# Performance work log

Measured on AMD Instinct MI355X. Metric: run time of the kernel, lower is better.

Reference implementation:

```python
import jax, jax.numpy as jnp
import numpy as np

K = 3; PAD = 1; STRIDE = 1; EPS = 1e-5


def setup_inputs() -> dict:
    key = jax.random.key(0)
    k0, k1, k2 = jax.random.split(key, 3)
    B, C, H, W, O = 4, 256, 64, 64, 256
    x = jax.random.normal(k0, (B, C, H, W), jnp.float32)
    # offset conv: small random weights so offsets are nontrivial but bounded
    w_off = jax.random.normal(k1, (2 * K * K, C, K, K), jnp.float32) * 0.01
    b_off = jnp.zeros((2 * K * K,), jnp.float32)
    # kaiming normal, mode=fan_out: std = sqrt(2 / (O*K*K))
    w_def = jax.random.normal(k2, (O, C, K, K), jnp.float32) * np.float32(np.sqrt(2.0 / (O * K * K)))
    gamma = jnp.ones((O,), jnp.float32)
    beta = jnp.zeros((O,), jnp.float32)
    return {"x": x, "w_off": w_off, "b_off": b_off, "w_def": w_def, "gamma": gamma, "beta": beta}


def _bilinear_gather(x, py, px):
    """x: [B,C,H,W]; py,px: [B,K2,Ho,Wo] float sample coords.
    Returns [B,K2,Ho,Wo,C] with zero padding outside (per-corner masking,
    matching torchvision deform_conv2d)."""
    B, C, H, W = x.shape
    y0f = jnp.floor(py); x0f = jnp.floor(px)
    wy1 = py - y0f; wy0 = 1.0 - wy1
    wx1 = px - x0f; wx0 = 1.0 - wx1
    bidx = jnp.arange(B)[:, None, None, None]

    def corner(yf, xf, wgt):
        valid = (yf >= 0) & (yf <= H - 1) & (xf >= 0) & (xf <= W - 1)
        yc = jnp.clip(yf.astype(jnp.int32), 0, H - 1)
        xc = jnp.clip(xf.astype(jnp.int32), 0, W - 1)
        v = x[bidx, :, yc, xc]  # [B,K2,Ho,Wo,C] (advanced idx moves C last)
        return v * (wgt * valid)[..., None]

    return (corner(y0f, x0f, wy0 * wx0) + corner(y0f, x0f + 1.0, wy0 * wx1)
            + corner(y0f + 1.0, x0f, wy1 * wx0) + corner(y0f + 1.0, x0f + 1.0, wy1 * wx1))


def _forward(x, w_off, b_off, w_def, gamma, beta):
    B, C, H, W = x.shape
    O = w_def.shape[0]
    K2 = K * K
    # 1) offset-predicting conv
    off = jax.lax.conv_general_dilated(x, w_off, (STRIDE, STRIDE), ((PAD, PAD), (PAD, PAD)))
    off = off + b_off[None, :, None, None]
    Ho, Wo = off.shape[2], off.shape[3]
    off = off.reshape(B, K2, 2, Ho, Wo)  # pairs (dy, dx) per kernel tap
    # 2) deformable sampling locations
    ky, kx = jnp.meshgrid(jnp.arange(K, dtype=jnp.float32), jnp.arange(K, dtype=jnp.float32), indexing='ij')
    base_y = (jnp.arange(Ho, dtype=jnp.float32) * STRIDE - PAD)
    base_x = (jnp.arange(Wo, dtype=jnp.float32) * STRIDE - PAD)
    py = off[:, :, 0] + ky.reshape(K2)[None, :, None, None] + base_y[None, None, :, None]
    px = off[:, :, 1] + kx.reshape(K2)[None, :, None, None] + base_x[None, None, None, :]
    vals = _bilinear_gather(x, py, px)  # [B,K2,Ho,Wo,C]
    # 3) deform conv GEMM (bias=False)
    out = jnp.einsum('bkhwc,ock->bohw', vals, w_def.reshape(O, C, K2))
    # 4) BatchNorm (training mode: batch stats) + ReLU
    mean = out.mean(axis=(0, 2, 3))
    var = out.var(axis=(0, 2, 3))
    out = (out - mean[None, :, None, None]) * (gamma * jax.lax.rsqrt(var + EPS))[None, :, None, None]
    out = out + beta[None, :, None, None]
    return jax.nn.relu(out)


def reference(x, w_off, b_off, w_def, gamma, beta):
    return _forward(x, w_off, b_off, w_def, gamma, beta)
```

## Files before the change

kernel.cpp:

```cpp
#include <hip/hip_runtime.h>
#include <hip/hip_bf16.h>

typedef unsigned int  uint;
typedef unsigned short ushort;
typedef short bf16x8 __attribute__((ext_vector_type(8)));
typedef float f32x4  __attribute__((ext_vector_type(4)));

#define HW   4096
#define KD   2304

__device__ __forceinline__ void load_lds16(const void* g, void* l) {
    __builtin_amdgcn_global_load_lds((const __attribute__((address_space(1))) void*)g,
                                     (__attribute__((address_space(3))) void*)l, 16, 0, 0);
}
__device__ __forceinline__ float blo(uint u) { return __uint_as_float(u << 16); }
__device__ __forceinline__ float bhi(uint u) { return __uint_as_float(u & 0xffff0000u); }
__device__ __forceinline__ uint pack2(float e, float o) {
    __hip_bfloat16 he = __float2bfloat16(e), ho = __float2bfloat16(o);
    return (uint)(*(ushort*)&he) | ((uint)(*(ushort*)&ho) << 16);
}

__global__ void prep_x2(const float* __restrict__ x, uint* __restrict__ x2) {
    int idx = blockIdx.x * 256 + threadIdx.x;
    int a  = idx & 4095;
    int cp = (idx >> 12) & 127;
    int b  = idx >> 19;
    const float* p = x + ((size_t)(b * 256 + 2 * cp)) * HW + a;
    x2[idx] = pack2(p[0], p[HW]);
}

__global__ void prep_bt(const float* __restrict__ w_def, ushort* __restrict__ bt) {
    int idx = blockIdx.x * 256 + threadIdx.x;
    int c   = idx & 255;
    int tap = (idx >> 8) % 9;
    int o   = idx / KD;
    __hip_bfloat16 h = __float2bfloat16(w_def[(o * 256 + c) * 9 + tap]);
    bt[idx] = *(ushort*)&h;
}

__global__ void prep_bt0(const float* __restrict__ w_off, ushort* __restrict__ bt0) {
    int idx = blockIdx.x * 256 + threadIdx.x;
    int c   = idx & 255;
    int tap = (idx >> 8) % 9;
    int j   = idx / KD;
    float v = (j < 18) ? w_off[(j * 256 + c) * 9 + tap] : 0.f;
    __hip_bfloat16 h = __float2bfloat16(v);
    bt0[idx] = *(ushort*)&h;
}

__global__ __launch_bounds__(256) void gemm_off(const uint* __restrict__ x2,
                                                const ushort* __restrict__ bt0,
                                                const float* __restrict__ b_off,
                                                float* __restrict__ off) {
    int id = blockIdx.x;
    int xcd = id & 7;
    int b = xcd >> 1, h = (xcd & 1) * 32 + (id >> 3);
    int t = threadIdx.x, wv = t >> 6, lane = t & 63;
    int mrow = lane & 15, quad = lane >> 4;

    __shared__ uint   lX[3 * 32 * 64];
    __shared__ ushort lB[32 * 576];

    f32x4 acc[2];
    acc[0] = {0.f, 0.f, 0.f, 0.f};
    acc[1] = {0.f, 0.f, 0.f, 0.f};

    for (int cb = 0; cb < 4; ++cb) {
#pragma unroll
        for (int s = 0; s < 6; ++s) {
            int q  = s * 4 + wv;
            int dy = q >> 3;
            int y  = h + dy - 1;
            int dl = (q & 7) * 256 + lane * 4;
            int cp = dl >> 6, w4 = dl & 63;
            uint* dst = &lX[q * 256 + lane * 4];
            if ((unsigned)y < 64u) {
                const uint* src = x2 + ((size_t)(b * 128 + cb * 32 + cp)) * HW + y * 64 + w4;
                load_lds16(src, &lX[q * 256]);
            } else {
                uint4 z = {0u, 0u, 0u, 0u};
                *(uint4*)dst = z;
            }
        }
#pragma unroll
        for (int s = 0; s < 9; ++s) {
            int q = s * 4 + wv;
            int e = q * 512 + lane * 8;
            int o  = e / 576;
            int r  = e - o * 576;
            int chp = r >> 3;
            int ch  = chp ^ (o & 7);
            int tap = ch >> 3, k8 = ch & 7;
            const ushort* src = bt0 + (size_t)o * KD + tap * 256 + cb * 64 + k8 * 8;
            load_lds16(src, &lB[q * 512]);
        }
        __syncthreads();

#pragma unroll
        for (int tap = 0; tap < 9; ++tap) {
            int dy = tap / 3, dx = tap % 3;
            int xx = wv * 16 + mrow + dx - 1;
            bool vx = (unsigned)xx < 64u;
#pragma unroll
            for (int kb = 0; kb < 2; ++kb) {
                int cp0 = kb * 16 + quad * 4;
                uint ad[4];
#pragma unroll
                for (int i = 0; i < 4; ++i)
                    ad[i] = vx ? lX[(dy * 32 + cp0 + i) * 64 + xx] : 0u;
                bf16x8 af = *(bf16x8*)ad;
#pragma unroll
                for (int n = 0; n < 2; ++n) {
                    int o = n * 16 + mrow;
                    int chs = (tap * 8 + (((kb * 4 + quad)) ^ (o & 7)));
                    bf16x8 bfr = *(const bf16x8*)&lB[o * 576 + chs * 8];
                    acc[n] = __builtin_amdgcn_mfma_f32_16x16x32_bf16(af, bfr, acc[n], 0, 0, 0);
                }
            }
        }
        __syncthreads();
    }
#pragma unroll
    for (int n = 0; n < 2; ++n) {
        int o = n * 16 + mrow;
        float bias = (o < 18) ? b_off[o] : 0.f;
        f32x4 v = acc[n];
        v.x += bias; v.y += bias; v.z += bias; v.w += bias;
        int wpos = wv * 16 + quad * 4;
        *(f32x4*)(off + ((size_t)(b * 32 + o)) * HW + h * 64 + wpos) = v;
    }
}

__global__ __launch_bounds__(512) void fused_main(const uint* __restrict__ x2,
                                                  const ushort* __restrict__ bt,
                                                  const float* __restrict__ off,
                                                  float* __restrict__ out,
                                                  float* __restrict__ stats) {
    int id = blockIdx.x;
    int xcd = id & 7;
    int b = xcd >> 1, h = (xcd & 1) * 32 + (id >> 3);
    int t = threadIdx.x;
    int wv = t >> 6, lane = t & 63;
    int mrow = lane & 15, quad = lane >> 4;
    int w  = t & 63;
    int cq = (t >> 6) & 7;

    __shared__ int    sAc[4][9][64];
    __shared__ float  sWc[4][9][64];
    __shared__ ushort lA[2][64 * 64];
    __shared__ ushort lB[2][256 * 64];

    for (int i = t; i < 576; i += 512) {
        int tap = i >> 6, ww = i & 63;
        int hw = h * 64 + ww;
        float oy = off[((size_t)(b * 32 + 2 * tap)) * HW + hw];
        float ox = off[((size_t)(b * 32 + 2 * tap + 1)) * HW + hw];
        float py = oy + (float)(tap / 3 + h - 1);
        float px = ox + (float)(tap % 3 + ww - 1);
        float y0f = floorf(py), x0f = floorf(px);
        float wy1 = py - y0f, wx1 = px - x0f;
        float wy0 = 1.f - wy1, wx0 = 1.f - wx1;
        bool vy0 = (y0f >= 0.f) && (y0f <= 63.f);
        bool vy1 = (y0f >= -1.f) && (y0f <= 62.f);
        bool vx0 = (x0f >= 0.f) && (x0f <= 63.f);
        bool vx1 = (x0f >= -1.f) && (x0f <= 62.f);
        int iy0 = min(max((int)y0f, 0), 63),  iy1 = min(max((int)y0f + 1, 0), 63);
        int ix0 = min(max((int)x0f, 0), 63),  ix1 = min(max((int)x0f + 1, 0), 63);
        sAc[0][tap][ww] = iy0 * 64 + ix0;
        sAc[1][tap][ww] = iy0 * 64 + ix1;
        sAc[2][tap][ww] = iy1 * 64 + ix0;
        sAc[3][tap][ww] = iy1 * 64 + ix1;
        sWc[0][tap][ww] = wy0 * wx0 * (float)(vy0 && vx0);
        sWc[1][tap][ww] = wy0 * wx1 * (float)(vy0 && vx1);
        sWc[2][tap][ww] = wy1 * wx0 * (float)(vy1 && vx0);
        sWc[3][tap][ww] = wy1 * wx1 * (float)(vy1 && vx1);
    }
    __syncthreads();

    f32x4 acc[4][2];
#pragma unroll
    for (int m = 0; m < 4; ++m)
#pragma unroll
        for (int n = 0; n < 2; ++n) acc[m][n] = {0.f, 0.f, 0.f, 0.f};

    const uint* xb = x2 + (size_t)(b * 128) * HW;

    {
        int tap = 0, cb = 0;
        int a0 = sAc[0][tap][w], a1 = sAc[1][tap][w], a2 = sAc[2][tap][w], a3 = sAc[3][tap][w];
        float f0 = sWc[0][tap][w], f1 = sWc[1][tap][w], f2 = sWc[2][tap][w], f3 = sWc[3][tap][w];
        const uint* xp = xb + (size_t)(cb * 32 + cq * 4) * HW;
        uint r[4];
#pragma unroll
        for (int j = 0; j < 4; ++j) {
            const uint* p = xp + (size_t)j * HW;
            uint u0 = p[a0], u1 = p[a1], u2 = p[a2], u3 = p[a3];
            float e = f0 * blo(u0) + f1 * blo(u1) + f2 * blo(u2) + f3 * blo(u3);
            float o = f0 * bhi(u0) + f1 * bhi(u1) + f2 * bhi(u2) + f3 * bhi(u3);
            r[j] = pack2(e, o);
        }
        uint4 g = {r[0], r[1], r[2], r[3]};
        *(uint4*)&lA[0][w * 64 + ((cq ^ (w & 7)) * 8)] = g;
#pragma unroll
        for (int s2 = 0; s2 < 4; ++s2) {
            int e = s2 * 512 + t;
            int o = e >> 3, pp = e & 7;
            int k8 = pp ^ (o & 7);
            const ushort* src = bt + (size_t)o * KD + tap * 256 + cb * 64 + k8 * 8;
            load_lds16(src, &lB[0][(e & ~63) * 8]);
        }
    }

    int p = 0;
    for (int s = 0; s < 36; ++s) {
        __syncthreads();
        bool more = (s + 1) < 36;
        uint4 g;
        if (more) {
            int tap = (s + 1) >> 2, cb = (s + 1) & 3;
            int a0 = sAc[0][tap][w], a1 = sAc[1][tap][w], a2 = sAc[2][tap][w], a3 = sAc[3][tap][w];
            float f0 = sWc[0][tap][w], f1 = sWc[1][tap][w], f2 = sWc[2][tap][w], f3 = sWc[3][tap][w];
            const uint* xp = xb + (size_t)(cb * 32 + cq * 4) * HW;
            uint r[4];
#pragma unroll
            for (int j = 0; j < 4; ++j) {
                const uint* pq = xp + (size_t)j * HW;
                uint u0 = pq[a0], u1 = pq[a1], u2 = pq[a2], u3 = pq[a3];
                float e = f0 * blo(u0) + f1 * blo(u1) + f2 * blo(u2) + f3 * blo(u3);
                float o = f0 * bhi(u0) + f1 * bhi(u1) + f2 * bhi(u2) + f3 * bhi(u3);
                r[j] = pack2(e, o);
            }
            g = {r[0], r[1], r[2], r[3]};
#pragma unroll
            for (int s2 = 0; s2 < 4; ++s2) {
                int e = s2 * 512 + t;
                int o = e >> 3, pp = e & 7;
                int k8 = pp ^ (o & 7);
                const ushort* src = bt + (size_t)o * KD + tap * 256 + cb * 64 + k8 * 8;
                load_lds16(src, &lB[p ^ 1][(e & ~63) * 8]);
            }
        }
#pragma unroll
        for (int kb = 0; kb < 2; ++kb) {
            bf16x8 af[4];
#pragma unroll
            for (int m = 0; m < 4; ++m) {
                int r = m * 16 + mrow;
                af[m] = *(const bf16x8*)&lA[p][r * 64 + (((kb * 4 + quad) ^ (r & 7)) * 8)];
            }
#pragma unroll
            for (int n = 0; n < 2; ++n) {
                int r = wv * 32 + n * 16 + mrow;
                bf16x8 bfr = *(const bf16x8*)&lB[p][r * 64 + (((kb * 4 + quad) ^ (r & 7)) * 8)];
#pragma unroll
                for (int m = 0; m < 4; ++m)
                    acc[m][n] = __builtin_amdgcn_mfma_f32_16x16x32_bf16(af[m], bfr, acc[m][n], 0, 0, 0);
            }
        }
        if (more)
            *(uint4*)&lA[p ^ 1][w * 64 + ((cq ^ (w & 7)) * 8)] = g;
        p ^= 1;
    }

#pragma unroll
    for (int n = 0; n < 2; ++n) {
        int o = wv * 32 + n * 16 + mrow;
        float ss = 0.f, qq = 0.f;
#pragma unroll
        for (int m = 0; m < 4; ++m) {
            int pos = m * 16 + quad * 4;
            f32x4 v = acc[m][n];
            *(f32x4*)(out + ((size_t)(b * 256 + o)) * HW + h * 64 + pos) = v;
            ss += v.x + v.y + v.z + v.w;
            qq += v.x * v.x + v.y * v.y + v.z * v.z + v.w * v.w;
        }
        ss += __shfl_xor(ss, 16); ss += __shfl_xor(ss, 32);
        qq += __shfl_xor(qq, 16); qq += __shfl_xor(qq, 32);
        if (quad == 0) {
            atomicAdd(&stats[o], ss);
            atomicAdd(&stats[512 + o], qq);
        }
    }
}

__global__ void bn_finalize(const float* __restrict__ stats,
                            const float* __restrict__ gamma,
                            float* __restrict__ ms) {
    int o = threadIdx.x;
    float S = stats[o], S2 = stats[512 + o];
    float m  = S / 16384.f;
    float var = S2 / 16384.f - m * m;
    ms[o]       = m;
    ms[256 + o] = gamma[o] * rsqrtf(var + 1e-5f);
}

__global__ void bn_apply(float* __restrict__ out,
                         const float* __restrict__ ms,
                         const float* __restrict__ beta) {
    int idx4 = blockIdx.x * 256 + threadIdx.x;
    int o = (idx4 >> 10) & 255;
    float4 v = ((const float4*)out)[idx4];
    float mu = ms[o], sc = ms[256 + o], be = beta[o];
    v.x = fmaxf((v.x - mu) * sc + be, 0.f);
    v.y = fmaxf((v.y - mu) * sc + be, 0.f);
    v.z = fmaxf((v.z - mu) * sc + be, 0.f);
    v.w = fmaxf((v.w - mu) * sc + be, 0.f);
    ((float4*)out)[idx4] = v;
}

extern "C" void kernel_launch(void* const* d_in, const int* in_sizes, int n_in,
                              void* d_out, int out_size, void* d_ws, size_t ws_size,
                              hipStream_t stream) {
    const float* x     = (const float*)d_in[0];
    const float* w_off = (const float*)d_in[1];
    const float* b_off = (const float*)d_in[2];
    const float* w_def = (const float*)d_in[3];
    const float* gamma = (const float*)d_in[4];
    const float* beta  = (const float*)d_in[5];
    float* out = (float*)d_out;

    char* ws = (char*)d_ws;
    uint*   x2    = (uint*)ws;
    ushort* bt    = (ushort*)(ws + 8388608);
    ushort* bt0   = (ushort*)(ws + 9568256);
    float*  off   = (float*)(ws + 9715712);
    float*  stats = (float*)(ws + 11812864);
    float*  ms    = (float*)(ws + 11816960);

    hipMemsetAsync(stats, 0, 4096, stream);
    prep_x2 <<<8192, 256, 0, stream>>>(x, x2);
    prep_bt <<<2304, 256, 0, stream>>>(w_def, bt);
    prep_bt0<<<288,  256, 0, stream>>>(w_off, bt0);
    gemm_off<<<256, 256, 0, stream>>>(x2, bt0, b_off, off);
    fused_main<<<256, 512, 0, stream>>>(x2, bt, off, out, stats);
    bn_finalize<<<1, 256, 0, stream>>>(stats, gamma, ms);
    bn_apply<<<4096, 256, 0, stream>>>(out, ms, beta);
}
```

Baseline: 174.9 us.

## Warp-specialize deformable GEMM into producer and MFMA consumer waves

The main fused kernel goes from 512 to 1024 threads and splits its waves by role. Eight producer waves do the bilinear gather and the async weight-tile loads into double-buffered LDS, while eight consumer waves run only the MFMA loop, so gathering and matrix math overlap instead of alternating within each wave. The offset-conv kernel also doubles its threads so each wave computes one 16x16 output tile instead of two, for more parallelism. This adds a larger block with tighter register limits, and the consumers still wait on the same per-stage barrier as the producers.

After: 179.9 us. 1.03x slower.

```diff
diff --git a/kernel.cpp b/kernel.cpp
--- a/kernel.cpp
+++ b/kernel.cpp
@@ -48,7 +48,7 @@
     bt0[idx] = *(ushort*)&h;
 }
 
-__global__ __launch_bounds__(256) void gemm_off(const uint* __restrict__ x2,
+__global__ __launch_bounds__(512) void gemm_off(const uint* __restrict__ x2,
                                                 const ushort* __restrict__ bt0,
                                                 const float* __restrict__ b_off,
                                                 float* __restrict__ off) {
@@ -57,18 +57,17 @@
     int b = xcd >> 1, h = (xcd & 1) * 32 + (id >> 3);
     int t = threadIdx.x, wv = t >> 6, lane = t & 63;
     int mrow = lane & 15, quad = lane >> 4;
+    int mq = wv & 3, nn = wv >> 2;
 
     __shared__ uint   lX[3 * 32 * 64];
     __shared__ ushort lB[32 * 576];
 
-    f32x4 acc[2];
-    acc[0] = {0.f, 0.f, 0.f, 0.f};
-    acc[1] = {0.f, 0.f, 0.f, 0.f};
+    f32x4 acc = {0.f, 0.f, 0.f, 0.f};
 
     for (int cb = 0; cb < 4; ++cb) {
 #pragma unroll
-        for (int s = 0; s < 6; ++s) {
-            int q  = s * 4 + wv;
+        for (int s = 0; s < 3; ++s) {
+            int q  = s * 8 + wv;
             int dy = q >> 3;
             int y  = h + dy - 1;
             int dl = (q & 7) * 256 + lane * 4;
@@ -83,23 +82,25 @@
             }
         }
 #pragma unroll
-        for (int s = 0; s < 9; ++s) {
-            int q = s * 4 + wv;
-            int e = q * 512 + lane * 8;
-            int o  = e / 576;
-            int r  = e - o * 576;
-            int chp = r >> 3;
-            int ch  = chp ^ (o & 7);
-            int tap = ch >> 3, k8 = ch & 7;
-            const ushort* src = bt0 + (size_t)o * KD + tap * 256 + cb * 64 + k8 * 8;
-            load_lds16(src, &lB[q * 512]);
+        for (int s = 0; s < 5; ++s) {
+            int q = s * 8 + wv;
+            if (q < 36) {
+                int e = q * 512 + lane * 8;
+                int o  = e / 576;
+                int r  = e - o * 576;
+                int chp = r >> 3;
+                int ch  = chp ^ (o & 7);
+                int tap = ch >> 3, k8 = ch & 7;
+                const ushort* src = bt0 + (size_t)o * KD + tap * 256 + cb * 64 + k8 * 8;
+                load_lds16(src, &lB[q * 512]);
+            }
         }
         __syncthreads();
 
 #pragma unroll
         for (int tap = 0; tap < 9; ++tap) {
             int dy = tap / 3, dx = tap % 3;
-            int xx = wv * 16 + mrow + dx - 1;
+            int xx = mq * 16 + mrow + dx - 1;
             bool vx = (unsigned)xx < 64u;
 #pragma unroll
             for (int kb = 0; kb < 2; ++kb) {
@@ -109,39 +110,36 @@
                 for (int i = 0; i < 4; ++i)
                     ad[i] = vx ? lX[(dy * 32 + cp0 + i) * 64 + xx] : 0u;
                 bf16x8 af = *(bf16x8*)ad;
-#pragma unroll
-                for (int n = 0; n < 2; ++n) {
-                    int o = n * 16 + mrow;
-                    int chs = (tap * 8 + (((kb * 4 + quad)) ^ (o & 7)));
-                    bf16x8 bfr = *(const bf16x8*)&lB[o * 576 + chs * 8];
-                    acc[n] = __builtin_amdgcn_mfma_f32_16x16x32_bf16(af, bfr, acc[n], 0, 0, 0);
-                }
+                int o = nn * 16 + mrow;
+                int chs = (tap * 8 + (((kb * 4 + quad)) ^ (o & 7)));
+                bf16x8 bfr = *(const bf16x8*)&lB[o * 576 + chs * 8];
+                acc = __builtin_amdgcn_mfma_f32_16x16x32_bf16(af, bfr, acc, 0, 0, 0);
             }
         }
         __syncthreads();
     }
-#pragma unroll
-    for (int n = 0; n < 2; ++n) {
-        int o = n * 16 + mrow;
+    {
+        int o = nn * 16 + mrow;
         float bias = (o < 18) ? b_off[o] : 0.f;
-        f32x4 v = acc[n];
+        f32x4 v = acc;
         v.x += bias; v.y += bias; v.z += bias; v.w += bias;
-        int wpos = wv * 16 + quad * 4;
+        int wpos = mq * 16 + quad * 4;
         *(f32x4*)(off + ((size_t)(b * 32 + o)) * HW + h * 64 + wpos) = v;
     }
 }
 
-__global__ __launch_bounds__(512) void fused_main(const uint* __restrict__ x2,
-                                                  const ushort* __restrict__ bt,
-                                                  const float* __restrict__ off,
-                                                  float* __restrict__ out,
-                                                  float* __restrict__ stats) {
+__global__ __launch_bounds__(1024, 4) void fused_main(const uint* __restrict__ x2,
+                                                      const ushort* __restrict__ bt,
+                                                      const float* __restrict__ off,
+                                                      float* __restrict__ out,
+                                                      float* __restrict__ stats) {
     int id = blockIdx.x;
     int xcd = id & 7;
     int b = xcd >> 1, h = (xcd & 1) * 32 + (id >> 3);
     int t = threadIdx.x;
     int wv = t >> 6, lane = t & 63;
     int mrow = lane & 15, quad = lane >> 4;
+    bool producer = (wv < 8);
     int w  = t & 63;
     int cq = (t >> 6) & 7;
 
@@ -150,7 +148,7 @@
     __shared__ ushort lA[2][64 * 64];
     __shared__ ushort lB[2][256 * 64];
 
-    for (int i = t; i < 576; i += 512) {
+    for (int i = t; i < 576; i += 1024) {
         int tap = i >> 6, ww = i & 63;
         int hw = h * 64 + ww;
         float oy = off[((size_t)(b * 32 + 2 * tap)) * HW + hw];
@@ -185,100 +183,86 @@
 
     const uint* xb = x2 + (size_t)(b * 128) * HW;
 
-    {
-        int tap = 0, cb = 0;
+    auto stage = [&](int sl, ushort* lAb, ushort* lBb) {
+        int tap = sl >> 2, cb = sl & 3;
         int a0 = sAc[0][tap][w], a1 = sAc[1][tap][w], a2 = sAc[2][tap][w], a3 = sAc[3][tap][w];
         float f0 = sWc[0][tap][w], f1 = sWc[1][tap][w], f2 = sWc[2][tap][w], f3 = sWc[3][tap][w];
         const uint* xp = xb + (size_t)(cb * 32 + cq * 4) * HW;
-        uint r[4];
+        uint u0[4], u1[4], u2[4], u3[4];
 #pragma unroll
         for (int j = 0; j < 4; ++j) {
-            const uint* p = xp + (size_t)j * HW;
-            uint u0 = p[a0], u1 = p[a1], u2 = p[a2], u3 = p[a3];
-            float e = f0 * blo(u0) + f1 * blo(u1) + f2 * blo(u2) + f3 * blo(u3);
-            float o = f0 * bhi(u0) + f1 * bhi(u1) + f2 * bhi(u2) + f3 * bhi(u3);
-            r[j] = pack2(e, o);
-        }
-        uint4 g = {r[0], r[1], r[2], r[3]};
-        *(uint4*)&lA[0][w * 64 + ((cq ^ (w & 7)) * 8)] = g;
+            const uint* pq = xp + (size_t)j * HW;
+            u0[j] = pq[a0]; u1[j] = pq[a1]; u2[j] = pq[a2]; u3[j] = pq[a3];
+        }
 #pragma unroll
         for (int s2 = 0; s2 < 4; ++s2) {
             int e = s2 * 512 + t;
             int o = e >> 3, pp = e & 7;
             int k8 = pp ^ (o & 7);
             const ushort* src = bt + (size_t)o * KD + tap * 256 + cb * 64 + k8 * 8;
-            load_lds16(src, &lB[0][(e & ~63) * 8]);
-        }
-    }
+            load_lds16(src, &lBb[(e & ~63) * 8]);
+        }
+        uint r[4];
+#pragma unroll
+        for (int j = 0; j < 4; ++j) {
+            float ev = f0 * blo(u0[j]) + f1 * blo(u1[j]) + f2 * blo(u2[j]) + f3 * blo(u3[j]);
+            float ov = f0 * bhi(u0[j]) + f1 * bhi(u1[j]) + f2 * bhi(u2[j]) + f3 * bhi(u3[j]);
+            r[j] = pack2(ev, ov);
+        }
+        uint4 g = {r[0], r[1], r[2], r[3]};
+        *(uint4*)&lAb[w * 64 + ((cq ^ (w & 7)) * 8)] = g;
+    };
+
+    if (producer) stage(0, lA[0], lB[0]);
 
     int p = 0;
     for (int s = 0; s < 36; ++s) {
         __syncthreads();
-        bool more = (s + 1) < 36;
-        uint4 g;
-        if (more) {
-            int tap = (s + 1) >> 2, cb = (s + 1) & 3;
-            int a0 = sAc[0][tap][w], a1 = sAc[1][tap][w], a2 = sAc[2][tap][w], a3 = sAc[3][tap][w];
-            float f0 = sWc[0][tap][w], f1 = sWc[1][tap][w], f2 = sWc[2][tap][w], f3 = sWc[3][tap][w];
-            const uint* xp = xb + (size_t)(cb * 32 + cq * 4) * HW;
-            uint r[4];
-#pragma unroll
-            for (int j = 0; j < 4; ++j) {
-                const uint* pq = xp + (size_t)j * HW;
-                uint u0 = pq[a0], u1 = pq[a1], u2 = pq[a2], u3 = pq[a3];
-                float e = f0 * blo(u0) + f1 * blo(u1) + f2 * blo(u2) + f3 * blo(u3);
-                float o = f0 * bhi(u0) + f1 * bhi(u1) + f2 * bhi(u2) + f3 * bhi(u3);
-                r[j] = pack2(e, o);
-            }
-            g = {r[0], r[1], r[2], r[3]};
-#pragma unroll
-            for (int s2 = 0; s2 < 4; ++s2) {
-                int e = s2 * 512 + t;
-                int o = e >> 3, pp = e & 7;
-                int k8 = pp ^ (o & 7);
-                const ushort* src = bt + (size_t)o * KD + tap * 256 + cb * 64 + k8 * 8;
-                load_lds16(src, &lB[p ^ 1][(e & ~63) * 8]);
-            }
-        }
-#pragma unroll
-        for (int kb = 0; kb < 2; ++kb) {
-            bf16x8 af[4];
+        if (producer) {
+            if (s + 1 < 36) stage(s + 1, lA[p ^ 1], lB[p ^ 1]);
+        } else {
+            int wvc = wv - 8;
+#pragma unroll
+            for (int kb = 0; kb < 2; ++kb) {
+                bf16x8 af[4];
+#pragma unroll
+                for (int m = 0; m < 4; ++m) {
+                    int r = m * 16 + mrow;
+                    af[m] = *(const bf16x8*)&lA[p][r * 64 + (((kb * 4 + quad) ^ (r & 7)) * 8)];
+                }
+#pragma unroll
+                for (int n = 0; n < 2; ++n) {
+                    int r = wvc * 32 + n * 16 + mrow;
+                    bf16x8 bfr = *(const bf16x8*)&lB[p][r * 64 + (((kb * 4 + quad) ^ (r & 7)) * 8)];
+#pragma unroll
+                    for (int m = 0; m < 4; ++m)
+                        acc[m][n] = __builtin_amdgcn_mfma_f32_16x16x32_bf16(af[m], bfr, acc[m][n], 0, 0, 0);
+                }
+            }
+        }
+        p ^= 1;
+    }
+
+    if (!producer) {
+        int wvc = wv - 8;
+#pragma unroll
+        for (int n = 0; n < 2; ++n) {
+            int o = wvc * 32 + n * 16 + mrow;
+            float ss = 0.f, qq = 0.f;
 #pragma unroll
             for (int m = 0; m < 4; ++m) {
-                int r = m * 16 + mrow;
-                af[m] = *(const bf16x8*)&lA[p][r * 64 + (((kb * 4 + quad) ^ (r & 7)) * 8)];
-            }
-#pragma unroll
-            for (int n = 0; n < 2; ++n) {
-                int r = wv * 32 + n * 16 + mrow;
-                bf16x8 bfr = *(const bf16x8*)&lB[p][r * 64 + (((kb * 4 + quad) ^ (r & 7)) * 8)];
-#pragma unroll
-                for (int m = 0; m < 4; ++m)
-                    acc[m][n] = __builtin_amdgcn_mfma_f32_16x16x32_bf16(af[m], bfr, acc[m][n], 0, 0, 0);
-            }
-        }
-        if (more)
-            *(uint4*)&lA[p ^ 1][w * 64 + ((cq ^ (w & 7)) * 8)] = g;
-        p ^= 1;
-    }
-
-#pragma unroll
-    for (int n = 0; n < 2; ++n) {
-        int o = wv * 32 + n * 16 + mrow;
-        float ss = 0.f, qq = 0.f;
-#pragma unroll
-        for (int m = 0; m < 4; ++m) {
-            int pos = m * 16 + quad * 4;
-            f32x4 v = acc[m][n];
-            *(f32x4*)(out + ((size_t)(b * 256 + o)) * HW + h * 64 + pos) = v;
-            ss += v.x + v.y + v.z + v.w;
-            qq += v.x * v.x + v.y * v.y + v.z * v.z + v.w * v.w;
-        }
-        ss += __shfl_xor(ss, 16); ss += __shfl_xor(ss, 32);
-        qq += __shfl_xor(qq, 16); qq += __shfl_xor(qq, 32);
-        if (quad == 0) {
-            atomicAdd(&stats[o], ss);
-            atomicAdd(&stats[512 + o], qq);
+                int pos = m * 16 + quad * 4;
+                f32x4 v = acc[m][n];
+                *(f32x4*)(out + ((size_t)(b * 256 + o)) * HW + h * 64 + pos) = v;
+                ss += v.x + v.y + v.z + v.w;
+                qq += v.x * v.x + v.y * v.y + v.z * v.z + v.w * v.w;
+            }
+            ss += __shfl_xor(ss, 16); ss += __shfl_xor(ss, 32);
+            qq += __shfl_xor(qq, 16); qq += __shfl_xor(qq, 32);
+            if (quad == 0) {
+                atomicAdd(&stats[o], ss);
+                atomicAdd(&stats[512 + o], qq);
+            }
         }
     }
 }
@@ -331,8 +315,8 @@
     prep_x2 <<<8192, 256, 0, stream>>>(x, x2);
     prep_bt <<<2304, 256, 0, stream>>>(w_def, bt);
     prep_bt0<<<288,  256, 0, stream>>>(w_off, bt0);
-    gemm_off<<<256, 256, 0, stream>>>(x2, bt0, b_off, off);
-    fused_main<<<256, 512, 0, stream>>>(x2, bt, off, out, stats);
+    gemm_off<<<256, 512, 0, stream>>>(x2, bt0, b_off, off);
+    fused_main<<<256, 1024, 0, stream>>>(x2, bt, off, out, stats);
     bn_finalize<<<1, 256, 0, stream>>>(stats, gamma, ms);
     bn_apply<<<4096, 256, 0, stream>>>(out, ms, beta);
 }
```
